# Optimization experiments

Hardware: AMD Instinct MI355X
Metric: run time of the kernel (lower is better)

The kernel has to match this reference:

```python
import jax, jax.numpy as jnp
import numpy as np

N_NODES = 100000
N_EDGES = 1600000
IN_FEATS = 128
NUM_HEADS = 4
OUT_FEATS = 32
NEG_SLOPE = 0.2


def setup_inputs() -> dict:
    key = jax.random.key(0)
    k1, k2, k3, k4, k5, k6 = jax.random.split(key, 6)
    feat = jax.random.normal(k1, (N_NODES, IN_FEATS), dtype=jnp.float32)
    src = jax.random.randint(k2, (N_EDGES,), 0, N_NODES, dtype=jnp.int32)
    dst = jnp.sort(jax.random.randint(k3, (N_EDGES,), 0, N_NODES, dtype=jnp.int32))
    # glorot-style scale ~ VarianceScaling(sqrt(2), fan_avg)
    w_scale = np.sqrt(2.0 * 2.0 / (IN_FEATS + NUM_HEADS * OUT_FEATS)).astype(np.float32)
    a_scale = np.sqrt(2.0 * 2.0 / (1 + OUT_FEATS)).astype(np.float32)
    W = jax.random.normal(k4, (IN_FEATS, NUM_HEADS * OUT_FEATS), dtype=jnp.float32) * w_scale
    attn_l = jax.random.normal(k5, (NUM_HEADS, OUT_FEATS), dtype=jnp.float32) * a_scale
    attn_r = jax.random.normal(k6, (NUM_HEADS, OUT_FEATS), dtype=jnp.float32) * a_scale
    return {"feat": feat, "src": src, "dst": dst, "W": W, "attn_l": attn_l, "attn_r": attn_r}


def reference(feat, src, dst, W, attn_l, attn_r):
    # Linear projection: [N, H, D]
    ft = (feat @ W).reshape(-1, NUM_HEADS, OUT_FEATS)
    # Per-node attention halves: [N, H]
    el = jnp.einsum("nhd,hd->nh", ft, attn_l)
    er = jnp.einsum("nhd,hd->nh", ft, attn_r)
    # Edge scores: e_ij = LeakyReLU(el[src] + er[dst])  -> [E, H]
    e = el[src] + er[dst]
    e = jnp.where(e > 0, e, NEG_SLOPE * e)
    # edge_softmax: per-destination segment softmax over incoming edges
    emax = jax.ops.segment_max(e, dst, num_segments=N_NODES)  # [N, H]
    ex = jnp.exp(e - emax[dst])                               # [E, H]
    esum = jax.ops.segment_sum(ex, dst, num_segments=N_NODES)  # [N, H]
    a = ex / esum[dst]                                         # [E, H]
    # Weighted scatter-sum aggregation: sum_j a_ij * W h_j -> [N, H, D]
    m = ft[src] * a[:, :, None]
    out = jax.ops.segment_sum(m, dst, num_segments=N_NODES)
    return out
```

## Files before the change

### kernel.cpp

```cpp
#include <hip/hip_runtime.h>

#define N_NODES 100000
#define N_EDGES 1600000
#define NUM_HEADS 4
#define NEG_SLOPE 0.2f
#define LDSTRIDE 136
#define SEG_BLOCKS 1563

typedef __attribute__((ext_vector_type(8))) short bf16x8;
typedef __attribute__((ext_vector_type(4))) float f32x4;

__device__ __forceinline__ unsigned short f2bf(float x) {
    union { float f; unsigned u; } v; v.f = x;
    unsigned r = v.u + 0x7fffu + ((v.u >> 16) & 1u);
    return (unsigned short)(r >> 16);
}
__device__ __forceinline__ unsigned short f2h(float x) {
    union { _Float16 h; unsigned short u; } v; v.h = (_Float16)x;
    return v.u;
}

__global__ __launch_bounds__(256) void prep_seg_kernel(
    const int* __restrict__ dst, int* __restrict__ seg,
    const float* __restrict__ W, const float* __restrict__ attn_l,
    const float* __restrict__ attn_r, unsigned short* __restrict__ Wt2)
{
    const int b = blockIdx.x;
    if (b < SEG_BLOCKS) {
        int i4 = b * 256 + threadIdx.x;
        if (i4 >= N_EDGES / 4) return;
        const int e0 = 4 * i4;
        const int4 d = ((const int4*)dst)[i4];
        const int dp = (e0 == 0) ? -1 : dst[e0 - 1];
        for (int n = dp + 1; n <= d.x; ++n) seg[n] = e0;
        for (int n = d.x + 1; n <= d.y; ++n) seg[n] = e0 + 1;
        for (int n = d.y + 1; n <= d.z; ++n) seg[n] = e0 + 2;
        for (int n = d.z + 1; n <= d.w; ++n) seg[n] = e0 + 3;
        if (e0 + 4 == N_EDGES)
            for (int n = d.w + 1; n <= N_NODES; ++n) seg[n] = N_EDGES;
    } else {
        int idx = (b - SEG_BLOCKS) * 256 + threadIdx.x;
        if (idx >= 136 * 128) return;
        int n = idx >> 7, k = idx & 127;
        if (n < 128) {
            Wt2[idx] = f2bf(W[k * 128 + n]);
        } else {
            int h = (n - 128) & 3;
            const float* av = ((n - 128) < 4 ? attn_l : attn_r) + h * 32;
            const float* col = W + k * 128 + h * 32;
            float s = 0.f;
#pragma unroll
            for (int d2 = 0; d2 < 32; ++d2) s += col[d2] * av[d2];
            Wt2[idx] = f2bf(s);
        }
    }
}

__global__ __launch_bounds__(256, 3) void gemm_kernel(
    const float* __restrict__ feat, const unsigned short* __restrict__ Wt2,
    unsigned short* __restrict__ ft, float* __restrict__ el,
    float* __restrict__ er)
{
    __shared__ __align__(16) unsigned short B_lds[136 * LDSTRIDE];
    const int t = threadIdx.x;
    const int nbase = blockIdx.x * 128;
    const int w = t >> 6, lane = t & 63;
    const int l15 = lane & 15, quad = lane >> 4;

    int g0 = nbase + w * 32 + l15;      if (g0 >= N_NODES) g0 = N_NODES - 1;
    int g1 = nbase + w * 32 + 16 + l15; if (g1 >= N_NODES) g1 = N_NODES - 1;
    const float4* f40 = (const float4*)feat + (size_t)g0 * 32 + quad * 2;
    const float4* f41 = (const float4*)feat + (size_t)g1 * 32 + quad * 2;
    float4 fr0[8], fr1[8];
#pragma unroll
    for (int ks = 0; ks < 4; ++ks) {
        fr0[2 * ks] = f40[ks * 8]; fr0[2 * ks + 1] = f40[ks * 8 + 1];
        fr1[2 * ks] = f41[ks * 8]; fr1[2 * ks + 1] = f41[ks * 8 + 1];
    }

    {
        const int4* Wt4 = (const int4*)Wt2;
#pragma unroll
        for (int i = 0; i < 9; ++i) {
            int idx = t + 256 * i;
            if (idx < 2176) {
                int n = idx >> 4, cg = idx & 15;
                *(int4*)(&B_lds[n * LDSTRIDE + cg * 8]) = Wt4[idx];
            }
        }
    }
    __syncthreads();

    bf16x8 a0[4], a1[4];
#pragma unroll
    for (int ks = 0; ks < 4; ++ks) {
        float4 fa = fr0[2 * ks], fb = fr0[2 * ks + 1];
        a0[ks][0] = (short)f2bf(fa.x); a0[ks][1] = (short)f2bf(fa.y);
        a0[ks][2] = (short)f2bf(fa.z); a0[ks][3] = (short)f2bf(fa.w);
        a0[ks][4] = (short)f2bf(fb.x); a0[ks][5] = (short)f2bf(fb.y);
        a0[ks][6] = (short)f2bf(fb.z); a0[ks][7] = (short)f2bf(fb.w);
        fa = fr1[2 * ks]; fb = fr1[2 * ks + 1];
        a1[ks][0] = (short)f2bf(fa.x); a1[ks][1] = (short)f2bf(fa.y);
        a1[ks][2] = (short)f2bf(fa.z); a1[ks][3] = (short)f2bf(fa.w);
        a1[ks][4] = (short)f2bf(fb.x); a1[ks][5] = (short)f2bf(fb.y);
        a1[ks][6] = (short)f2bf(fb.z); a1[ks][7] = (short)f2bf(fb.w);
    }

    f32x4 acc0[9], acc1[9];
#pragma unroll
    for (int c = 0; c < 9; ++c) {
        acc0[c] = (f32x4){0.f, 0.f, 0.f, 0.f};
        acc1[c] = (f32x4){0.f, 0.f, 0.f, 0.f};
    }

    const unsigned short* Brow = &B_lds[l15 * LDSTRIDE + quad * 8];
    const unsigned short* Brow8 = &B_lds[(128 + (l15 & 7)) * LDSTRIDE + quad * 8];
#pragma unroll
    for (int ks = 0; ks < 4; ++ks) {
#pragma unroll
        for (int c = 0; c < 8; ++c) {
            bf16x8 b = *(const bf16x8*)(Brow + (c * 16) * LDSTRIDE + ks * 32);
            acc0[c] = __builtin_amdgcn_mfma_f32_16x16x32_bf16(a0[ks], b, acc0[c], 0, 0, 0);
            acc1[c] = __builtin_amdgcn_mfma_f32_16x16x32_bf16(a1[ks], b, acc1[c], 0, 0, 0);
        }
        bf16x8 b8 = *(const bf16x8*)(Brow8 + ks * 32);
        acc0[8] = __builtin_amdgcn_mfma_f32_16x16x32_bf16(a0[ks], b8, acc0[8], 0, 0, 0);
        acc1[8] = __builtin_amdgcn_mfma_f32_16x16x32_bf16(a1[ks], b8, acc1[8], 0, 0, 0);
    }

#pragma unroll
    for (int reg = 0; reg < 4; ++reg) {
        const int ga = nbase + w * 32 + quad * 4 + reg;
        if (ga < N_NODES) {
            if (l15 < 4)      el[ga * 4 + l15] = acc0[8][reg];
            else if (l15 < 8) er[ga * 4 + (l15 - 4)] = acc0[8][reg];
        }
        const int gb = ga + 16;
        if (gb < N_NODES) {
            if (l15 < 4)      el[gb * 4 + l15] = acc1[8][reg];
            else if (l15 < 8) er[gb * 4 + (l15 - 4)] = acc1[8][reg];
        }
    }

    __syncthreads();
#pragma unroll
    for (int c = 0; c < 8; ++c) {
#pragma unroll
        for (int reg = 0; reg < 4; ++reg) {
            B_lds[(w * 32 + quad * 4 + reg) * LDSTRIDE + c * 16 + l15] =
                f2h(acc0[c][reg]);
            B_lds[(w * 32 + 16 + quad * 4 + reg) * LDSTRIDE + c * 16 + l15] =
                f2h(acc1[c][reg]);
        }
    }
    __syncthreads();

#pragma unroll
    for (int i = 0; i < 8; ++i) {
        int idx = t + 256 * i;
        int node = idx >> 4, cg = idx & 15;
        int gg = nbase + node;
        if (gg < N_NODES) {
            int4 val = *(const int4*)(&B_lds[node * LDSTRIDE + cg * 8]);
            *(int4*)(&ft[(size_t)gg * 128 + cg * 8]) = val;
        }
    }
}

__global__ __launch_bounds__(256) void aggregate_kernel(
    const unsigned short* __restrict__ ft, const float* __restrict__ el,
    const float* __restrict__ er, const int* __restrict__ src,
    const int* __restrict__ seg, float* __restrict__ out)
{
    const int node = blockIdx.x * 4 + (threadIdx.x >> 6);
    if (node >= N_NODES) return;
    const int lane = threadIdx.x & 63;
    const int qt = lane >> 4;
    const int l15 = lane & 15;
    const int hf = l15 >> 2;

    const int beg = __builtin_amdgcn_readfirstlane(seg[node]);
    const int end = __builtin_amdgcn_readfirstlane(seg[node + 1]);
    const float er_h = er[node * 4 + hf];

    float dpart = 0.f;
    float4 accA = make_float4(0.f, 0.f, 0.f, 0.f);
    float4 accB = make_float4(0.f, 0.f, 0.f, 0.f);

    for (int c0 = beg; c0 < end; c0 += 16) {
        const int cb = c0 + 4 * qt;
        int s4[4];
#pragma unroll
        for (int k = 0; k < 4; ++k) {
            int ci = cb + k;
            s4[k] = src[ci < end ? ci : end - 1];
        }
        float ev[4];
#pragma unroll
        for (int k = 0; k < 4; ++k) ev[k] = el[s4[k] * 4 + hf];
        float p[4];
#pragma unroll
        for (int k = 0; k < 4; ++k) {
            float e = ev[k] + er_h;
            e = (e > 0.f) ? e : NEG_SLOPE * e;
            p[k] = (cb + k < end) ? __expf(e) : 0.f;
            dpart += p[k];
        }
        uint4 v[4];
#pragma unroll
        for (int k = 0; k < 4; ++k)
            v[k] = *(const uint4*)(ft + (((size_t)(unsigned)s4[k]) << 7) + l15 * 8);
#pragma unroll
        for (int k = 0; k < 4; ++k) {
            const float pj = p[k];
            asm("v_fma_mix_f32 %0, %2, %3, %0 op_sel_hi:[1,0,0]\n\t"
                "v_fma_mix_f32 %1, %2, %3, %1 op_sel:[1,0,0] op_sel_hi:[1,0,0]"
                : "+v"(accA.x), "+v"(accA.y) : "v"(v[k].x), "v"(pj));
            asm("v_fma_mix_f32 %0, %2, %3, %0 op_sel_hi:[1,0,0]\n\t"
                "v_fma_mix_f32 %1, %2, %3, %1 op_sel:[1,0,0] op_sel_hi:[1,0,0]"
                : "+v"(accA.z), "+v"(accA.w) : "v"(v[k].y), "v"(pj));
            asm("v_fma_mix_f32 %0, %2, %3, %0 op_sel_hi:[1,0,0]\n\t"
                "v_fma_mix_f32 %1, %2, %3, %1 op_sel:[1,0,0] op_sel_hi:[1,0,0]"
                : "+v"(accB.x), "+v"(accB.y) : "v"(v[k].z), "v"(pj));
            asm("v_fma_mix_f32 %0, %2, %3, %0 op_sel_hi:[1,0,0]\n\t"
                "v_fma_mix_f32 %1, %2, %3, %1 op_sel:[1,0,0] op_sel_hi:[1,0,0]"
                : "+v"(accB.z), "+v"(accB.w) : "v"(v[k].w), "v"(pj));
        }
    }

    dpart  += __shfl_xor(dpart, 16);
    accA.x += __shfl_xor(accA.x, 16); accA.y += __shfl_xor(accA.y, 16);
    accA.z += __shfl_xor(accA.z, 16); accA.w += __shfl_xor(accA.w, 16);
    accB.x += __shfl_xor(accB.x, 16); accB.y += __shfl_xor(accB.y, 16);
    accB.z += __shfl_xor(accB.z, 16); accB.w += __shfl_xor(accB.w, 16);
    dpart  += __shfl_xor(dpart, 32);
    accA.x += __shfl_xor(accA.x, 32); accA.y += __shfl_xor(accA.y, 32);
    accA.z += __shfl_xor(accA.z, 32); accA.w += __shfl_xor(accA.w, 32);
    accB.x += __shfl_xor(accB.x, 32); accB.y += __shfl_xor(accB.y, 32);
    accB.z += __shfl_xor(accB.z, 32); accB.w += __shfl_xor(accB.w, 32);

    const float inv = (dpart > 0.f) ? 1.f / dpart : 0.f;

    if (qt == 0) {
        float4 o0 = make_float4(accA.x * inv, accA.y * inv, accA.z * inv, accA.w * inv);
        float4 o1 = make_float4(accB.x * inv, accB.y * inv, accB.z * inv, accB.w * inv);
        float* op = out + (size_t)node * 128 + l15 * 8;
        *(float4*)op = o0;
        *(float4*)(op + 4) = o1;
    }
}

extern "C" void kernel_launch(void* const* d_in, const int* in_sizes, int n_in,
                              void* d_out, int out_size, void* d_ws, size_t ws_size,
                              hipStream_t stream) {
    const float* feat   = (const float*)d_in[0];
    const int*   src    = (const int*)d_in[1];
    const int*   dst    = (const int*)d_in[2];
    const float* W      = (const float*)d_in[3];
    const float* attn_l = (const float*)d_in[4];
    const float* attn_r = (const float*)d_in[5];
    float* out = (float*)d_out;

    unsigned short* ft = (unsigned short*)d_ws;
    float* el  = (float*)(ft + (size_t)12800000);
    float* er  = el + 400000;
    unsigned short* Wt2 = (unsigned short*)(er + 400000);
    int* seg = (int*)(Wt2 + 136 * 128);

    prep_seg_kernel<<<SEG_BLOCKS + 68, 256, 0, stream>>>(
        dst, seg, W, attn_l, attn_r, Wt2);
    gemm_kernel<<<(N_NODES + 127) / 128, 256, 0, stream>>>(feat, Wt2, ft, el, er);
    aggregate_kernel<<<(N_NODES + 3) / 4, 256, 0, stream>>>(
        ft, el, er, src, seg, out);
}
```

Baseline: 192.4 us.

## Fuse three stages into one cooperative persistent kernel with grid syncs

Replaces the three launches (segment/weight prep, GEMM, aggregation) with a single cooperative kernel of 768 persistent blocks that runs each stage in grid-stride loops separated by grid.sync(). This removes two launch boundaries and their tail drain. Aggregation output now uses nontemporal stores. In exchange, the aggregation phase loses occupancy because it is held to launch_bounds(256,3) with a large LDS allocation. Grid syncs add cost, and the old three-kernel path remains as a fallback if the cooperative launch fails.

```diff
diff --git a/kernel.cpp b/kernel.cpp
--- a/kernel.cpp
+++ b/kernel.cpp
@@ -1,11 +1,16 @@
 #include <hip/hip_runtime.h>
+#include <hip/hip_cooperative_groups.h>
+
+namespace cg = cooperative_groups;
 
 #define N_NODES 100000
 #define N_EDGES 1600000
-#define NUM_HEADS 4
 #define NEG_SLOPE 0.2f
 #define LDSTRIDE 136
+#define GEMM_BLOCKS 782
 #define SEG_BLOCKS 1563
+#define COOP_BLOCKS 768
+#define COOP_THREADS (COOP_BLOCKS * 256)
 
 typedef __attribute__((ext_vector_type(8))) short bf16x8;
 typedef __attribute__((ext_vector_type(4))) float f32x4;
@@ -20,50 +25,47 @@
     return v.u;
 }
 
-__global__ __launch_bounds__(256) void prep_seg_kernel(
-    const int* __restrict__ dst, int* __restrict__ seg,
-    const float* __restrict__ W, const float* __restrict__ attn_l,
+
+__device__ __forceinline__ void prep_item(
+    int idx, const float* __restrict__ W, const float* __restrict__ attn_l,
     const float* __restrict__ attn_r, unsigned short* __restrict__ Wt2)
 {
-    const int b = blockIdx.x;
-    if (b < SEG_BLOCKS) {
-        int i4 = b * 256 + threadIdx.x;
-        if (i4 >= N_EDGES / 4) return;
-        const int e0 = 4 * i4;
-        const int4 d = ((const int4*)dst)[i4];
-        const int dp = (e0 == 0) ? -1 : dst[e0 - 1];
-        for (int n = dp + 1; n <= d.x; ++n) seg[n] = e0;
-        for (int n = d.x + 1; n <= d.y; ++n) seg[n] = e0 + 1;
-        for (int n = d.y + 1; n <= d.z; ++n) seg[n] = e0 + 2;
-        for (int n = d.z + 1; n <= d.w; ++n) seg[n] = e0 + 3;
-        if (e0 + 4 == N_EDGES)
-            for (int n = d.w + 1; n <= N_NODES; ++n) seg[n] = N_EDGES;
+    if (idx >= 136 * 128) return;
+    int n = idx >> 7, k = idx & 127;
+    if (n < 128) {
+        Wt2[idx] = f2bf(W[k * 128 + n]);
     } else {
-        int idx = (b - SEG_BLOCKS) * 256 + threadIdx.x;
-        if (idx >= 136 * 128) return;
-        int n = idx >> 7, k = idx & 127;
-        if (n < 128) {
-            Wt2[idx] = f2bf(W[k * 128 + n]);
-        } else {
-            int h = (n - 128) & 3;
-            const float* av = ((n - 128) < 4 ? attn_l : attn_r) + h * 32;
-            const float* col = W + k * 128 + h * 32;
-            float s = 0.f;
-#pragma unroll
-            for (int d2 = 0; d2 < 32; ++d2) s += col[d2] * av[d2];
-            Wt2[idx] = f2bf(s);
-        }
-    }
-}
-
-__global__ __launch_bounds__(256, 3) void gemm_kernel(
+        int h = (n - 128) & 3;
+        const float* av = ((n - 128) < 4 ? attn_l : attn_r) + h * 32;
+        const float* col = W + k * 128 + h * 32;
+        float s = 0.f;
+#pragma unroll
+        for (int d2 = 0; d2 < 32; ++d2) s += col[d2] * av[d2];
+        Wt2[idx] = f2bf(s);
+    }
+}
+
+__device__ __forceinline__ void seg_item(
+    int i4, const int* __restrict__ dst, int* __restrict__ seg)
+{
+    const int e0 = 4 * i4;
+    const int4 d = ((const int4*)dst)[i4];
+    const int dp = (e0 == 0) ? -1 : dst[e0 - 1];
+    for (int n = dp + 1; n <= d.x; ++n) seg[n] = e0;
+    for (int n = d.x + 1; n <= d.y; ++n) seg[n] = e0 + 1;
+    for (int n = d.y + 1; n <= d.z; ++n) seg[n] = e0 + 2;
+    for (int n = d.z + 1; n <= d.w; ++n) seg[n] = e0 + 3;
+    if (e0 + 4 == N_EDGES)
+        for (int n = d.w + 1; n <= N_NODES; ++n) seg[n] = N_EDGES;
+}
+
+__device__ __forceinline__ void gemm_tile(
+    int tile, unsigned short* B_lds, int t,
     const float* __restrict__ feat, const unsigned short* __restrict__ Wt2,
     unsigned short* __restrict__ ft, float* __restrict__ el,
     float* __restrict__ er)
 {
-    __shared__ __align__(16) unsigned short B_lds[136 * LDSTRIDE];
-    const int t = threadIdx.x;
-    const int nbase = blockIdx.x * 128;
+    const int nbase = tile * 128;
     const int w = t >> 6, lane = t & 63;
     const int l15 = lane & 15, quad = lane >> 4;
 
@@ -84,8 +86,8 @@
         for (int i = 0; i < 9; ++i) {
             int idx = t + 256 * i;
             if (idx < 2176) {
-                int n = idx >> 4, cg = idx & 15;
-                *(int4*)(&B_lds[n * LDSTRIDE + cg * 8]) = Wt4[idx];
+                int n = idx >> 4, cg2 = idx & 15;
+                *(int4*)(&B_lds[n * LDSTRIDE + cg2 * 8]) = Wt4[idx];
             }
         }
     }
@@ -158,23 +160,21 @@
 #pragma unroll
     for (int i = 0; i < 8; ++i) {
         int idx = t + 256 * i;
-        int node = idx >> 4, cg = idx & 15;
+        int node = idx >> 4, cg2 = idx & 15;
         int gg = nbase + node;
         if (gg < N_NODES) {
-            int4 val = *(const int4*)(&B_lds[node * LDSTRIDE + cg * 8]);
-            *(int4*)(&ft[(size_t)gg * 128 + cg * 8]) = val;
-        }
-    }
-}
-
-__global__ __launch_bounds__(256) void aggregate_kernel(
+            int4 val = *(const int4*)(&B_lds[node * LDSTRIDE + cg2 * 8]);
+            *(int4*)(&ft[(size_t)gg * 128 + cg2 * 8]) = val;
+        }
+    }
+}
+
+__device__ __forceinline__ void agg_node(
+    int node, int lane,
     const unsigned short* __restrict__ ft, const float* __restrict__ el,
     const float* __restrict__ er, const int* __restrict__ src,
     const int* __restrict__ seg, float* __restrict__ out)
 {
-    const int node = blockIdx.x * 4 + (threadIdx.x >> 6);
-    if (node >= N_NODES) return;
-    const int lane = threadIdx.x & 63;
     const int qt = lane >> 4;
     const int l15 = lane & 15;
     const int hf = l15 >> 2;
@@ -242,12 +242,74 @@
     const float inv = (dpart > 0.f) ? 1.f / dpart : 0.f;
 
     if (qt == 0) {
-        float4 o0 = make_float4(accA.x * inv, accA.y * inv, accA.z * inv, accA.w * inv);
-        float4 o1 = make_float4(accB.x * inv, accB.y * inv, accB.z * inv, accB.w * inv);
+        f32x4 o0 = {accA.x * inv, accA.y * inv, accA.z * inv, accA.w * inv};
+        f32x4 o1 = {accB.x * inv, accB.y * inv, accB.z * inv, accB.w * inv};
         float* op = out + (size_t)node * 128 + l15 * 8;
-        *(float4*)op = o0;
-        *(float4*)(op + 4) = o1;
-    }
+        __builtin_nontemporal_store(o0, (f32x4*)op);
+        __builtin_nontemporal_store(o1, (f32x4*)(op + 4));
+    }
+}
+
+__global__ __launch_bounds__(256, 3) void fused_kernel(
+    const float* __restrict__ feat, const int* __restrict__ src,
+    const int* __restrict__ dst, const float* __restrict__ W,
+    const float* __restrict__ attn_l, const float* __restrict__ attn_r,
+    float* __restrict__ out, unsigned short* __restrict__ ft,
+    float* __restrict__ el, float* __restrict__ er,
+    unsigned short* __restrict__ Wt2, int* __restrict__ seg)
+{
+    __shared__ __align__(16) unsigned short B_lds[136 * LDSTRIDE];
+    cg::grid_group grid = cg::this_grid();
+    const int t = threadIdx.x;
+    const int gtid = blockIdx.x * 256 + t;
+
+    prep_item(gtid, W, attn_l, attn_r, Wt2);
+    for (int i4 = gtid; i4 < N_EDGES / 4; i4 += COOP_THREADS)
+        seg_item(i4, dst, seg);
+    grid.sync();
+
+    for (int tile = blockIdx.x; tile < GEMM_BLOCKS; tile += COOP_BLOCKS) {
+        gemm_tile(tile, B_lds, t, feat, Wt2, ft, el, er);
+        __syncthreads();
+    }
+    grid.sync();
+
+    const int wv = t >> 6, lane = t & 63;
+    for (int it = blockIdx.x; it < N_NODES / 4; it += COOP_BLOCKS)
+        agg_node(it * 4 + wv, lane, ft, el, er, src, seg, out);
+}
+
+__global__ __launch_bounds__(256) void fb_prep_seg_kernel(
+    const int* __restrict__ dst, int* __restrict__ seg,
+    const float* __restrict__ W, const float* __restrict__ attn_l,
+    const float* __restrict__ attn_r, unsigned short* __restrict__ Wt2)
+{
+    const int b = blockIdx.x;
+    if (b < SEG_BLOCKS) {
+        int i4 = b * 256 + threadIdx.x;
+        if (i4 < N_EDGES / 4) seg_item(i4, dst, seg);
+    } else {
+        prep_item((b - SEG_BLOCKS) * 256 + threadIdx.x, W, attn_l, attn_r, Wt2);
+    }
+}
+
+__global__ __launch_bounds__(256, 3) void fb_gemm_kernel(
+    const float* __restrict__ feat, const unsigned short* __restrict__ Wt2,
+    unsigned short* __restrict__ ft, float* __restrict__ el,
+    float* __restrict__ er)
+{
+    __shared__ __align__(16) unsigned short B_lds[136 * LDSTRIDE];
+    gemm_tile(blockIdx.x, B_lds, threadIdx.x, feat, Wt2, ft, el, er);
+}
+
+__global__ __launch_bounds__(256) void fb_aggregate_kernel(
+    const unsigned short* __restrict__ ft, const float* __restrict__ el,
+    const float* __restrict__ er, const int* __restrict__ src,
+    const int* __restrict__ seg, float* __restrict__ out)
+{
+    const int node = blockIdx.x * 4 + (threadIdx.x >> 6);
+    if (node >= N_NODES) return;
+    agg_node(node, threadIdx.x & 63, ft, el, er, src, seg, out);
 }
 
 extern "C" void kernel_launch(void* const* d_in, const int* in_sizes, int n_in,
@@ -267,9 +329,19 @@
     unsigned short* Wt2 = (unsigned short*)(er + 400000);
     int* seg = (int*)(Wt2 + 136 * 128);
 
-    prep_seg_kernel<<<SEG_BLOCKS + 68, 256, 0, stream>>>(
-        dst, seg, W, attn_l, attn_r, Wt2);
-    gemm_kernel<<<(N_NODES + 127) / 128, 256, 0, stream>>>(feat, Wt2, ft, el, er);
-    aggregate_kernel<<<(N_NODES + 3) / 4, 256, 0, stream>>>(
-        ft, el, er, src, seg, out);
-}
+    void* args[] = {
+        (void*)&feat, (void*)&src, (void*)&dst, (void*)&W,
+        (void*)&attn_l, (void*)&attn_r, (void*)&out, (void*)&ft,
+        (void*)&el, (void*)&er, (void*)&Wt2, (void*)&seg,
+    };
+    hipError_t err = hipLaunchCooperativeKernel(
+        (const void*)fused_kernel, dim3(COOP_BLOCKS), dim3(256), args, 0, stream);
+    if (err != hipSuccess) {
+        (void)hipGetLastError();
+        fb_prep_seg_kernel<<<SEG_BLOCKS + 68, 256, 0, stream>>>(
+            dst, seg, W, attn_l, attn_r, Wt2);
+        fb_gemm_kernel<<<GEMM_BLOCKS, 256, 0, stream>>>(feat, Wt2, ft, el, er);
+        fb_aggregate_kernel<<<(N_NODES + 3) / 4, 256, 0, stream>>>(
+            ft, el, er, src, seg, out);
+    }
+}
```

After: 381.2 us. 98.1% more time.
